# Optimization experiments

Hardware: AMD Instinct MI355X
Metric: run time of the kernel (lower is better)

## Reference

```python
import jax, jax.numpy as jnp
import numpy as np

POS_W = 1.0
ANG_W = 1.0
WID_W = 1.0
N = 1048560  # predictions (divisible by 17)
M = 8388480  # total GT grasps = sum(arange(N) % 17)


def setup_inputs() -> dict:
    key = jax.random.key(0)
    k1, k2 = jax.random.split(key)
    pred = jax.random.normal(k1, (N, 6), dtype=jnp.float32)
    all_targets = jax.random.normal(k2, (M, 6), dtype=jnp.float32)
    # ragged counts in [0, 16]; sum == M exactly
    target_counts = (jnp.arange(N, dtype=jnp.int64) % 17)
    return {"pred": pred, "all_targets": all_targets, "target_counts": target_counts}


def _smooth_l1(x):
    a = jnp.abs(x)
    return jnp.where(a < 1.0, 0.5 * x * x, a - 0.5)


def reference(pred, all_targets, target_counts):
    n = pred.shape[0]
    m = all_targets.shape[0]
    # segment id for each GT row (contiguous slices, order of target_counts)
    seg = jnp.repeat(jnp.arange(n), target_counts, total_repeat_length=m)  # (M,)
    p = pred[seg]  # (M,6) gathered predictions
    dp = p[:, :2] - all_targets[:, :2]
    da = p[:, 2:4] - all_targets[:, 2:4]
    dw = p[:, 4] - all_targets[:, 4]
    dist = (POS_W * jnp.sum(dp * dp, axis=-1)
            + ANG_W * jnp.sum(da * da, axis=-1)
            + WID_W * dw * dw)  # (M,)
    # ragged argmin per segment (first occurrence, like torch.argmin)
    min_d = jax.ops.segment_min(dist, seg, num_segments=n)  # (N,)
    row = jnp.arange(m)
    cand = jnp.where(dist == min_d[seg], row, m)
    arg = jax.ops.segment_min(cand, seg, num_segments=n)  # (N,) global row idx or m
    has = target_counts > 0
    gt = all_targets[jnp.where(has, jnp.clip(arg, 0, m - 1), 0)]  # (N,6)
    # fused per-prediction loss against the closest GT
    loss_pos = jnp.sum(_smooth_l1(pred[:, :2] - gt[:, :2]), axis=-1)
    loss_ang = jnp.sum(jnp.abs(pred[:, 2:4] - gt[:, 2:4]), axis=-1)
    loss_wid = _smooth_l1(pred[:, 4] - gt[:, 4])
    losses = jnp.where(has, POS_W * loss_pos + ANG_W * loss_ang + WID_W * loss_wid, 0.0)
    return jnp.mean(losses)  # reduction='mean'
```

## Files before the change

### kernel.cpp

```cpp
#include <hip/hip_runtime.h>
#include <math.h>

#define POS_W 1.0f
#define ANG_W 1.0f
#define WID_W 1.0f
#define CHUNK 1024

__device__ __forceinline__ float smooth_l1(float x) {
    float a = fabsf(x);
    return a < 1.0f ? 0.5f * x * x : a - 0.5f;
}

__global__ void k_block_sums(const int* __restrict__ counts, int stride, int n,
                             int* __restrict__ blockSums) {
    int i = blockIdx.x * 256 + threadIdx.x;
    int c = (i < n) ? counts[(long long)i * stride] : 0;
    for (int off = 32; off > 0; off >>= 1) c += __shfl_down(c, off, 64);
    __shared__ int sdata[4];
    int lane = threadIdx.x & 63, wave = threadIdx.x >> 6;
    if (lane == 0) sdata[wave] = c;
    __syncthreads();
    if (threadIdx.x == 0)
        blockSums[blockIdx.x] = sdata[0] + sdata[1] + sdata[2] + sdata[3];
}

__global__ void k_scan_blocks(const int* __restrict__ blockSums, int nb,
                              int* __restrict__ blockOffs) {
    int t = threadIdx.x;
    int per = (nb + 255) / 256;
    int start = t * per;
    int end = min(start + per, nb);
    int sum = 0;
    for (int j = start; j < end; ++j) sum += blockSums[j];
    __shared__ int s[256];
    s[t] = sum;
    __syncthreads();
    for (int d = 1; d < 256; d <<= 1) {
        int v = (t >= d) ? s[t - d] : 0;
        __syncthreads();
        s[t] += v;
        __syncthreads();
    }
    int run = s[t] - sum;
    for (int j = start; j < end; ++j) {
        blockOffs[j] = run;
        run += blockSums[j];
    }
}

__global__ __launch_bounds__(256) void k_loss(
    const float* __restrict__ pred, const float* __restrict__ tgt,
    const int* __restrict__ counts, int stride, int n,
    const int* __restrict__ blockOffs, float invN, float* __restrict__ out) {
    __shared__ int s[256];
    __shared__ float2 ch[CHUNK * 3];

    int t = threadIdx.x;
    int i = blockIdx.x * 256 + t;
    int c = (i < n) ? counts[(long long)i * stride] : 0;

    s[t] = c;
    __syncthreads();
    for (int d = 1; d < 256; d <<= 1) {
        int v = (t >= d) ? s[t - d] : 0;
        __syncthreads();
        s[t] += v;
        __syncthreads();
    }
    int off = s[t] - c;
    int total = s[255];
    int winStart = blockOffs[blockIdx.x];

    bool active = (i < n) && (c > 0);
    float p0 = 0, p1 = 0, p2 = 0, p3 = 0, p4 = 0;
    if (active) {
        const float2* p2p = (const float2*)(pred + (long long)i * 6);
        float2 a = p2p[0], b = p2p[1], w = p2p[2];
        p0 = a.x; p1 = a.y; p2 = b.x; p3 = b.y; p4 = w.x;
    }

    float best = INFINITY;
    float b0 = 0, b1 = 0, b2 = 0, b3 = 0, b4 = 0;

    const float2* tgt2 = (const float2*)tgt;
    for (int base = 0; base < total; base += CHUNK) {
        int rows = min(CHUNK, total - base);
        const float2* src = tgt2 + (long long)(winStart + base) * 3;
        for (int k = t; k < rows * 3; k += 256) ch[k] = src[k];
        __syncthreads();
        if (active) {
            int lo = max(off, base), hi = min(off + c, base + rows);
            for (int r = lo; r < hi; ++r) {
                int l3 = (r - base) * 3;
                float2 ga = ch[l3], gb = ch[l3 + 1], gw = ch[l3 + 2];
                float d0 = p0 - ga.x, d1 = p1 - ga.y;
                float d2 = p2 - gb.x, d3 = p3 - gb.y;
                float d4 = p4 - gw.x;
                float dist = POS_W * (d0 * d0 + d1 * d1) +
                             ANG_W * (d2 * d2 + d3 * d3) + WID_W * d4 * d4;
                if (dist < best) {
                    best = dist;
                    b0 = ga.x; b1 = ga.y; b2 = gb.x; b3 = gb.y; b4 = gw.x;
                }
            }
        }
        __syncthreads();
    }

    float loss = 0.0f;
    if (active) {
        loss = POS_W * (smooth_l1(p0 - b0) + smooth_l1(p1 - b1)) +
               ANG_W * (fabsf(p2 - b2) + fabsf(p3 - b3)) +
               WID_W * smooth_l1(p4 - b4);
    }

    for (int o = 32; o > 0; o >>= 1) loss += __shfl_down(loss, o, 64);
    __shared__ float fs[4];
    int lane = t & 63, wave = t >> 6;
    if (lane == 0) fs[wave] = loss;
    __syncthreads();
    if (t == 0) {
        float tot = (fs[0] + fs[1] + fs[2] + fs[3]) * invN;
        atomicAdd(out, tot);
    }
}

extern "C" void kernel_launch(void* const* d_in, const int* in_sizes, int n_in,
                              void* d_out, int out_size, void* d_ws,
                              size_t ws_size, hipStream_t stream) {
    const float* pred = (const float*)d_in[0];
    const float* tgt = (const float*)d_in[1];
    const int* counts = (const int*)d_in[2];
    int n = in_sizes[0] / 6;
    int stride = (in_sizes[2] == n) ? 1 : 2;
    int nb = (n + 255) / 256;

    int* blockSums = (int*)d_ws;
    int* blockOffs = blockSums + nb;
    float* out = (float*)d_out;

    hipMemsetAsync(d_out, 0, sizeof(float), stream);
    k_block_sums<<<nb, 256, 0, stream>>>(counts, stride, n, blockSums);
    k_scan_blocks<<<1, 256, 0, stream>>>(blockSums, nb, blockOffs);
    k_loss<<<nb, 256, 0, stream>>>(pred, tgt, counts, stride, n, blockOffs,
                                   1.0f / n, out);
}
```

Measured before the change: 339.2 us.

## Prefetch next target chunk into registers and use wave-shuffle block scan

Replaces the shared-memory Hillis-Steele block scan, which needs many barriers, with a wave-level shuffle scan plus a 4-entry cross-wave combine. The target-chunk load now goes through registers as a software pipeline: the next chunk is loaded into registers (12 float2 per thread) while the current chunk is processed from LDS. The aim is to cut barrier overhead and hide global load latency, at the cost of higher register pressure.

Result: faster. 309.2 us (-8.8%).

```diff
diff --git a/kernel.cpp b/kernel.cpp
--- a/kernel.cpp
+++ b/kernel.cpp
@@ -5,6 +5,7 @@
 #define ANG_W 1.0f
 #define WID_W 1.0f
 #define CHUNK 1024
+#define F2PT 12
 
 __device__ __forceinline__ float smooth_l1(float x) {
     float a = fabsf(x);
@@ -52,23 +53,27 @@
     const float* __restrict__ pred, const float* __restrict__ tgt,
     const int* __restrict__ counts, int stride, int n,
     const int* __restrict__ blockOffs, float invN, float* __restrict__ out) {
-    __shared__ int s[256];
     __shared__ float2 ch[CHUNK * 3];
+    __shared__ int wsum[4];
+    __shared__ float fs[4];
 
     int t = threadIdx.x;
+    int lane = t & 63, wave = t >> 6;
     int i = blockIdx.x * 256 + t;
     int c = (i < n) ? counts[(long long)i * stride] : 0;
 
-    s[t] = c;
+    int incl = c;
+#pragma unroll
+    for (int d = 1; d < 64; d <<= 1) {
+        int v = __shfl_up(incl, d, 64);
+        if (lane >= d) incl += v;
+    }
+    if (lane == 63) wsum[wave] = incl;
     __syncthreads();
-    for (int d = 1; d < 256; d <<= 1) {
-        int v = (t >= d) ? s[t - d] : 0;
-        __syncthreads();
-        s[t] += v;
-        __syncthreads();
-    }
-    int off = s[t] - c;
-    int total = s[255];
+    int w0 = wsum[0], w1 = wsum[1], w2 = wsum[2], w3 = wsum[3];
+    int waveOff = (wave > 0 ? w0 : 0) + (wave > 1 ? w1 : 0) + (wave > 2 ? w2 : 0);
+    int off = waveOff + incl - c;
+    int total = w0 + w1 + w2 + w3;
     int winStart = blockOffs[blockIdx.x];
 
     bool active = (i < n) && (c > 0);
@@ -82,16 +87,41 @@
     float best = INFINITY;
     float b0 = 0, b1 = 0, b2 = 0, b3 = 0, b4 = 0;
 
-    const float2* tgt2 = (const float2*)tgt;
+    const float2* win = (const float2*)tgt + (long long)winStart * 3;
+    float2 r[F2PT];
+
+    {
+        int nF2 = min(CHUNK, total) * 3;
+#pragma unroll
+        for (int j = 0; j < F2PT; ++j) {
+            int k = t + 256 * j;
+            if (k < nF2) r[j] = win[k];
+        }
+    }
+
     for (int base = 0; base < total; base += CHUNK) {
         int rows = min(CHUNK, total - base);
-        const float2* src = tgt2 + (long long)(winStart + base) * 3;
-        for (int k = t; k < rows * 3; k += 256) ch[k] = src[k];
+        int nF2c = rows * 3;
+#pragma unroll
+        for (int j = 0; j < F2PT; ++j) {
+            int k = t + 256 * j;
+            if (k < nF2c) ch[k] = r[j];
+        }
         __syncthreads();
+        int nbase = base + CHUNK;
+        if (nbase < total) {
+            int nF2n = min(CHUNK, total - nbase) * 3;
+            const float2* srcn = win + (long long)nbase * 3;
+#pragma unroll
+            for (int j = 0; j < F2PT; ++j) {
+                int k = t + 256 * j;
+                if (k < nF2n) r[j] = srcn[k];
+            }
+        }
         if (active) {
             int lo = max(off, base), hi = min(off + c, base + rows);
-            for (int r = lo; r < hi; ++r) {
-                int l3 = (r - base) * 3;
+            for (int rr = lo; rr < hi; ++rr) {
+                int l3 = (rr - base) * 3;
                 float2 ga = ch[l3], gb = ch[l3 + 1], gw = ch[l3 + 2];
                 float d0 = p0 - ga.x, d1 = p1 - ga.y;
                 float d2 = p2 - gb.x, d3 = p3 - gb.y;
@@ -115,8 +145,6 @@
     }
 
     for (int o = 32; o > 0; o >>= 1) loss += __shfl_down(loss, o, 64);
-    __shared__ float fs[4];
-    int lane = t & 63, wave = t >> 6;
     if (lane == 0) fs[wave] = loss;
     __syncthreads();
     if (t == 0) {
```
